# Kernel optimization log

Hardware: AMD Instinct MI355X
Metric: run time of the kernel (lower is better)

Reference implementation:

```python
import jax, jax.numpy as jnp
import numpy as np

N_NODES = 50000
N_EDGES = 800000
NUM_RELS = 16
IN_DIM, H_DIM, OUT_DIM = 128, 128, 64


def setup_inputs() -> dict:
    key = jax.random.key(0)
    ks = jax.random.split(key, 7)
    feat = jax.random.normal(ks[0], (N_NODES, IN_DIM), dtype=jnp.float32)
    norm = jax.random.uniform(ks[1], (N_EDGES, 1), dtype=jnp.float32)
    bound1 = 1.0 / np.sqrt(IN_DIM)
    bound2 = 1.0 / np.sqrt(H_DIM)
    W1 = jax.random.uniform(ks[2], (NUM_RELS, IN_DIM, H_DIM), dtype=jnp.float32, minval=-bound1, maxval=bound1)
    W2 = jax.random.uniform(ks[3], (NUM_RELS, H_DIM, OUT_DIM), dtype=jnp.float32, minval=-bound2, maxval=bound2)
    src = jax.random.randint(ks[4], (N_EDGES,), 0, N_NODES, dtype=jnp.int32)
    dst = jax.random.randint(ks[5], (N_EDGES,), 0, N_NODES, dtype=jnp.int32)
    etypes = jax.random.randint(ks[6], (N_EDGES,), 0, NUM_RELS, dtype=jnp.int32)
    return {"feat": feat, "norm": norm, "W1": W1, "W2": W2, "src": src, "dst": dst, "etypes": etypes}


def _rgcn_layer(h, W, src, dst, etypes, norm, num_nodes):
    # Transform every node by every relation weight (dense batched GEMM),
    # then gather the (src, etype) slice per edge: identical math to
    # gather_mm(h[src], W, idx_b=etypes) since matmul commutes with gather.
    t = jnp.einsum('ni,rio->nro', h, W)          # [N, R, O]
    msg = t[src, etypes] * norm                  # [E, O]
    return jax.ops.segment_sum(msg, dst, num_segments=num_nodes)  # sum-aggregate


def reference(feat, norm, W1, W2, src, dst, etypes):
    n = feat.shape[0]
    h = jax.nn.relu(_rgcn_layer(feat, W1, src, dst, etypes, norm, n))
    out = _rgcn_layer(h, W2, src, dst, etypes, norm, n)
    return out
```

## Files before the change

kernel.cpp:

```cpp
#include <hip/hip_runtime.h>


#define R_NUM 16

typedef __attribute__((ext_vector_type(8))) short bf16x8;
typedef __attribute__((ext_vector_type(4))) float f32x4;

__device__ __forceinline__ float bf2f(unsigned short u) {
    unsigned int x = ((unsigned int)u) << 16;
    return __builtin_bit_cast(float, x);
}
__device__ __forceinline__ unsigned short f2bf(float f) {
    unsigned int x = __builtin_bit_cast(unsigned int, f);
    x += 0x7FFFu + ((x >> 16) & 1u);
    return (unsigned short)(x >> 16);
}
__device__ __forceinline__ unsigned pack2(float a, float b) {
    return (unsigned)f2bf(a) | ((unsigned)f2bf(b) << 16);
}
__device__ __forceinline__ float lo16(unsigned v) { return bf2f((unsigned short)(v & 0xFFFF)); }
__device__ __forceinline__ float hi16(unsigned v) { return bf2f((unsigned short)(v >> 16)); }

__global__ void detect_dtype(const unsigned short* __restrict__ raw, int* flag) {
    __shared__ int tot;
    if (threadIdx.x == 0) tot = 0;
    __syncthreads();
    int c = 0;
    for (int i = threadIdx.x; i < 4096; i += 256) {
        unsigned short u = raw[2 * i];
        int e = (u >> 7) & 0xFF;
        if (e >= 113 && e <= 134) c++;
    }
    atomicAdd(&tot, c);
    __syncthreads();
    if (threadIdx.x == 0) *flag = (tot > 2048) ? 1 : 0;
}

__global__ void transpose_both(const void* __restrict__ W1, const void* __restrict__ W2,
                               unsigned short* __restrict__ w1t, unsigned short* __restrict__ w2t,
                               const int* __restrict__ flagp) {
    const int flag = *flagp;
    const int n1 = R_NUM * 128 * 128;
    const int n2 = R_NUM * 128 * 64;
    int idx = blockIdx.x * 256 + threadIdx.x;
    if (idx < n1) {
        int k = idx % 128, o = (idx / 128) % 128, r = idx / (128 * 128);
        int iin = (r * 128 + k) * 128 + o;
        float v = flag ? bf2f(((const unsigned short*)W1)[iin]) : ((const float*)W1)[iin];
        w1t[idx] = f2bf(v);
    } else if (idx < n1 + n2) {
        int j = idx - n1;
        int k = j % 128, o = (j / 128) % 64, r = j / (128 * 64);
        int iin = (r * 128 + k) * 64 + o;
        float v = flag ? bf2f(((const unsigned short*)W2)[iin]) : ((const float*)W2)[iin];
        w2t[j] = f2bf(v);
    }
}

template <int NOUT, int AMODE>
__global__ __launch_bounds__(256, 3) void gemm_nb(const void* __restrict__ Asrc,
                                                  const unsigned short* __restrict__ Wt,
                                                  unsigned short* __restrict__ T, int nnodes,
                                                  const int* __restrict__ flagp) {
    constexpr int LDA = 136;
    constexpr int NTC = NOUT / 64;
    __shared__ unsigned short lA[64 * LDA];
    const int tid = threadIdx.x;
    const int node0 = blockIdx.x * 64;
    const int flag = (AMODE == 0) ? *flagp : 1;

    for (int i = tid; i < 64 * 16; i += 256) {
        int row = i >> 4, seg = i & 15;
        int node = node0 + row;
        uint4 v = make_uint4(0u, 0u, 0u, 0u);
        if (node < nnodes) {
            if (AMODE == 2 || flag) {
                v = *(const uint4*)((const unsigned short*)Asrc + (size_t)node * 128 + seg * 8);
            } else {
                const float* p = (const float*)Asrc + (size_t)node * 128 + seg * 8;
                float4 f0 = ((const float4*)p)[0];
                float4 f1 = ((const float4*)p)[1];
                v.x = pack2(f0.x, f0.y);
                v.y = pack2(f0.z, f0.w);
                v.z = pack2(f1.x, f1.y);
                v.w = pack2(f1.z, f1.w);
            }
        }
        *(uint4*)(lA + row * LDA + seg * 8) = v;
    }
    __syncthreads();

    const int w = tid >> 6, lane = tid & 63;
    const int quad = lane >> 4, mr = lane & 15;

    bf16x8 afr[16];
#pragma unroll
    for (int mt = 0; mt < 4; mt++)
#pragma unroll
        for (int kk = 0; kk < 4; kk++)
            afr[mt * 4 + kk] = *(const bf16x8*)(lA + (mt * 16 + mr) * LDA + kk * 32 + quad * 8);

    const unsigned short* wb = Wt + (size_t)(w * 16 + mr) * 128 + quad * 8;

    for (int rel = 0; rel < R_NUM; rel++) {
        const unsigned short* wr = wb + (size_t)rel * NOUT * 128;
        bf16x8 bf[NTC][4];
#pragma unroll
        for (int c = 0; c < NTC; c++)
#pragma unroll
            for (int kk = 0; kk < 4; kk++)
                bf[c][kk] = *(const bf16x8*)(wr + (size_t)c * 64 * 128 + kk * 32);

        f32x4 acc[4][NTC];
#pragma unroll
        for (int mt = 0; mt < 4; mt++)
#pragma unroll
            for (int c = 0; c < NTC; c++) acc[mt][c] = 0.f;

#pragma unroll
        for (int kk = 0; kk < 4; kk++)
#pragma unroll
            for (int c = 0; c < NTC; c++)
#pragma unroll
                for (int mt = 0; mt < 4; mt++)
                    acc[mt][c] = __builtin_amdgcn_mfma_f32_16x16x32_bf16(bf[c][kk],
                                                                         afr[mt * 4 + kk],
                                                                         acc[mt][c], 0, 0, 0);

#pragma unroll
        for (int mt = 0; mt < 4; mt++) {
            int node = node0 + mt * 16 + mr;
            if (node < nnodes) {
#pragma unroll
                for (int c = 0; c < NTC; c++) {
                    uint2 pv;
                    pv.x = pack2(acc[mt][c][0], acc[mt][c][1]);
                    pv.y = pack2(acc[mt][c][2], acc[mt][c][3]);
                    *(uint2*)(T + ((size_t)rel * nnodes + node) * NOUT + c * 64 + w * 16 +
                              quad * 4) = pv;
                }
            }
        }
    }
}

__global__ void hist_dst(const int* __restrict__ dst, int* __restrict__ counts, int nedges) {
    int e = blockIdx.x * 256 + threadIdx.x;
    if (e < nedges) atomicAdd(&counts[dst[e]], 1);
}

__global__ __launch_bounds__(256) void scan_phase1(const int* __restrict__ counts,
                                                   int* __restrict__ blocksums, int n) {
    __shared__ int red[256];
    int base = blockIdx.x * 1024 + threadIdx.x * 4;
    int s = 0;
#pragma unroll
    for (int j = 0; j < 4; j++) {
        int idx = base + j;
        if (idx < n) s += counts[idx];
    }
    red[threadIdx.x] = s;
    __syncthreads();
    for (int d = 128; d > 0; d >>= 1) {
        if (threadIdx.x < d) red[threadIdx.x] += red[threadIdx.x + d];
        __syncthreads();
    }
    if (threadIdx.x == 0) blocksums[blockIdx.x] = red[0];
}

__global__ __launch_bounds__(1024) void scan_phase2(const int* __restrict__ blocksums,
                                                    int* __restrict__ blockoff, int nb) {
    __shared__ int arr[1024];
    int t = threadIdx.x;
    arr[t] = (t < nb) ? blocksums[t] : 0;
    __syncthreads();
    for (int d = 1; d < 1024; d <<= 1) {
        int v = (t >= d) ? arr[t - d] : 0;
        __syncthreads();
        arr[t] += v;
        __syncthreads();
    }
    if (t < nb) blockoff[t] = (t == 0) ? 0 : arr[t - 1];
}

__global__ __launch_bounds__(256) void scan_phase3(const int* __restrict__ counts,
                                                   const int* __restrict__ blockoff,
                                                   int* __restrict__ offsets,
                                                   int* __restrict__ cursor, int n) {
    __shared__ int tsum[256];
    int base = blockIdx.x * 1024 + threadIdx.x * 4;
    int c[4];
    int s = 0;
#pragma unroll
    for (int j = 0; j < 4; j++) {
        int idx = base + j;
        c[j] = (idx < n) ? counts[idx] : 0;
        s += c[j];
    }
    tsum[threadIdx.x] = s;
    __syncthreads();
    for (int d = 1; d < 256; d <<= 1) {
        int v = (threadIdx.x >= d) ? tsum[threadIdx.x - d] : 0;
        __syncthreads();
        tsum[threadIdx.x] += v;
        __syncthreads();
    }
    int run = blockoff[blockIdx.x] + ((threadIdx.x == 0) ? 0 : tsum[threadIdx.x - 1]);
#pragma unroll
    for (int j = 0; j < 4; j++) {
        int idx = base + j;
        if (idx < n) {
            offsets[idx] = run;
            cursor[idx] = run;
            if (idx == n - 1) offsets[n] = run + c[j];
            run += c[j];
        }
    }
}

__global__ void fill_payload(const int* __restrict__ src, const int* __restrict__ dst,
                             const int* __restrict__ et, const void* __restrict__ nrm,
                             const int* __restrict__ flagp, int* __restrict__ cursor,
                             uint2* __restrict__ payload, int nedges) {
    int e = blockIdx.x * 256 + threadIdx.x;
    if (e >= nedges) return;
    int flag = *flagp;
    float nm = flag ? bf2f(((const unsigned short*)nrm)[e]) : ((const float*)nrm)[e];
    int pos = atomicAdd(&cursor[dst[e]], 1);
    uint2 pl;
    pl.x = ((unsigned)src[e] << 4) | (unsigned)(et[e] & 15);
    pl.y = __builtin_bit_cast(unsigned, nm);
    payload[pos] = pl;
}

template <int NOUT, int OUTMODE>
__global__ __launch_bounds__(256) void gather_seg(const unsigned short* __restrict__ T,
                                                  const int* __restrict__ offsets,
                                                  const uint2* __restrict__ payload,
                                                  void* __restrict__ out, int nnodes,
                                                  const int* __restrict__ flagp) {
    constexpr int SUBW = NOUT / 2;
    const int lane = threadIdx.x & 63;
    const int ll = lane & (SUBW - 1);
    const int dpb = 256 / SUBW;
    const int dst = blockIdx.x * dpb + threadIdx.x / SUBW;
    if (dst >= nnodes) return;
    const int base = lane & ~(SUBW - 1);
    const int beg = offsets[dst], end = offsets[dst + 1];
    float ax = 0.f, ay = 0.f;

    auto rowp = [&](unsigned key) {
        return (const unsigned*)(T + ((size_t)(key & 15) * nnodes + (key >> 4)) * NOUT);
    };

    for (int i = beg; i < end; i += SUBW) {
        int cnt = min(SUBW, end - i);
        uint2 pl = make_uint2(0u, 0u);
        if (ll < cnt) pl = payload[i + ll];
        int j = 0;
        for (; j + 4 <= cnt; j += 4) {
            unsigned k0 = (unsigned)__shfl((int)pl.x, base + j);
            unsigned k1 = (unsigned)__shfl((int)pl.x, base + j + 1);
            unsigned k2 = (unsigned)__shfl((int)pl.x, base + j + 2);
            unsigned k3 = (unsigned)__shfl((int)pl.x, base + j + 3);
            float n0 = __builtin_bit_cast(float, (unsigned)__shfl((int)pl.y, base + j));
            float n1 = __builtin_bit_cast(float, (unsigned)__shfl((int)pl.y, base + j + 1));
            float n2 = __builtin_bit_cast(float, (unsigned)__shfl((int)pl.y, base + j + 2));
            float n3 = __builtin_bit_cast(float, (unsigned)__shfl((int)pl.y, base + j + 3));
            unsigned v0 = rowp(k0)[ll];
            unsigned v1 = rowp(k1)[ll];
            unsigned v2 = rowp(k2)[ll];
            unsigned v3 = rowp(k3)[ll];
            ax = fmaf(lo16(v0), n0, ax); ay = fmaf(hi16(v0), n0, ay);
            ax = fmaf(lo16(v1), n1, ax); ay = fmaf(hi16(v1), n1, ay);
            ax = fmaf(lo16(v2), n2, ax); ay = fmaf(hi16(v2), n2, ay);
            ax = fmaf(lo16(v3), n3, ax); ay = fmaf(hi16(v3), n3, ay);
        }
        for (; j < cnt; j++) {
            unsigned k = (unsigned)__shfl((int)pl.x, base + j);
            float nm = __builtin_bit_cast(float, (unsigned)__shfl((int)pl.y, base + j));
            unsigned v = rowp(k)[ll];
            ax = fmaf(lo16(v), nm, ax);
            ay = fmaf(hi16(v), nm, ay);
        }
    }
    if (OUTMODE == 0) {
        ((unsigned*)out)[(size_t)dst * SUBW + ll] = pack2(fmaxf(ax, 0.f), fmaxf(ay, 0.f));
    } else {
        if (*flagp) {
            ((unsigned*)out)[(size_t)dst * SUBW + ll] = pack2(ax, ay);
        } else {
            float2 v;
            v.x = ax; v.y = ay;
            ((float2*)out)[(size_t)dst * SUBW + ll] = v;
        }
    }
}

template <int NOUT, int AMODE>
__global__ __launch_bounds__(256) void gemm_rel(const void* __restrict__ Asrc,
                                                const unsigned short* __restrict__ Wt,
                                                unsigned short* __restrict__ T, int nnodes,
                                                int rbase, const int* __restrict__ flagp) {
    constexpr int LDA = 136;
    __shared__ unsigned short lA[64 * LDA];
    __shared__ unsigned short lB[NOUT * LDA];
    const int tid = threadIdx.x;
    const int node0 = blockIdx.x * 64;
    const int rel = rbase + blockIdx.y;
    const int Gr = gridDim.y;
    const int flag = (AMODE == 0) ? *flagp : 1;

    for (int i = tid; i < 64 * 16; i += 256) {
        int row = i >> 4, seg = i & 15;
        int node = node0 + row;
        uint4 v = make_uint4(0u, 0u, 0u, 0u);
        if (node < nnodes) {
            if (AMODE == 1) {
                const float* p = (const float*)Asrc + (size_t)node * 128 + seg * 8;
                float4 f0 = ((const float4*)p)[0];
                float4 f1 = ((const float4*)p)[1];
                v.x = pack2(fmaxf(f0.x, 0.f), fmaxf(f0.y, 0.f));
                v.y = pack2(fmaxf(f0.z, 0.f), fmaxf(f0.w, 0.f));
                v.z = pack2(fmaxf(f1.x, 0.f), fmaxf(f1.y, 0.f));
                v.w = pack2(fmaxf(f1.z, 0.f), fmaxf(f1.w, 0.f));
            } else if (flag) {
                v = *(const uint4*)((const unsigned short*)Asrc + (size_t)node * 128 + seg * 8);
            } else {
                const float* p = (const float*)Asrc + (size_t)node * 128 + seg * 8;
                float4 f0 = ((const float4*)p)[0];
                float4 f1 = ((const float4*)p)[1];
                v.x = pack2(f0.x, f0.y);
                v.y = pack2(f0.z, f0.w);
                v.z = pack2(f1.x, f1.y);
                v.w = pack2(f1.z, f1.w);
            }
        }
        *(uint4*)(lA + row * LDA + seg * 8) = v;
    }
    for (int i = tid; i < NOUT * 16; i += 256) {
        int o = i >> 4, seg = i & 15;
        *(uint4*)(lB + o * LDA + seg * 8) =
            *(const uint4*)(Wt + ((size_t)rel * NOUT + o) * 128 + seg * 8);
    }
    __syncthreads();

    const int w = tid >> 6, lane = tid & 63;
    const int quad = lane >> 4, mr = lane & 15;
    constexpr int NT = NOUT / 16;
    f32x4 acc[NT];
#pragma unroll
    for (int t = 0; t < NT; t++) acc[t] = 0.f;
    const unsigned short* pa = lA + (w * 16 + mr) * LDA + quad * 8;
    const unsigned short* pb = lB + mr * LDA + quad * 8;
#pragma unroll
    for (int kk = 0; kk < 4; kk++) {
        bf16x8 a = *(const bf16x8*)(pa + kk * 32);
#pragma unroll
        for (int nt = 0; nt < NT; nt++) {
            bf16x8 b = *(const bf16x8*)(pb + nt * 16 * LDA + kk * 32);
            acc[nt] = __builtin_amdgcn_mfma_f32_16x16x32_bf16(a, b, acc[nt], 0, 0, 0);
        }
    }
#pragma unroll
    for (int nt = 0; nt < NT; nt++)
#pragma unroll
        for (int reg = 0; reg < 4; reg++) {
            int node = node0 + w * 16 + quad * 4 + reg;
            if (node < nnodes)
                T[((size_t)node * Gr + blockIdx.y) * NOUT + nt * 16 + mr] = f2bf(acc[nt][reg]);
        }
}

template <int NOUT>
__global__ void scatter_k(const unsigned short* __restrict__ T, int Gr, int rbase,
                          const void* __restrict__ nrm, const int* __restrict__ flagp,
                          const int* __restrict__ src, const int* __restrict__ dst,
                          const int* __restrict__ et, float* __restrict__ accum, int nedges) {
    constexpr int LPE = NOUT / 2;
    const int flag = *flagp;
    const int epb = 256 / LPE;
    const int sub = threadIdx.x % LPE;
    const int slot = threadIdx.x / LPE;
    for (int e = blockIdx.x * epb + slot; e < nedges; e += gridDim.x * epb) {
        int g = et[e] - rbase;
        if (g < 0 || g >= Gr) continue;
        int s = src[e], d = dst[e];
        float nm = flag ? bf2f(((const unsigned short*)nrm)[e]) : ((const float*)nrm)[e];
        unsigned pv = ((const unsigned*)(T + ((size_t)s * Gr + g) * NOUT))[sub];
        float* p = accum + (size_t)d * NOUT + sub * 2;
        unsafeAtomicAdd(p, lo16(pv) * nm);
        unsafeAtomicAdd(p + 1, hi16(pv) * nm);
    }
}

__global__ void write_out(const float* __restrict__ acc, void* __restrict__ dout, int n,
                          const int* __restrict__ flagp) {
    int flag = *flagp;
    int i = blockIdx.x * 256 + threadIdx.x;
    if (i >= n) return;
    float v = acc[i];
    if (flag) ((unsigned short*)dout)[i] = f2bf(v);
    else      ((float*)dout)[i] = v;
}

extern "C" void kernel_launch(void* const* d_in, const int* in_sizes, int n_in,
                              void* d_out, int out_size, void* d_ws, size_t ws_size,
                              hipStream_t stream) {
    const void* feat = d_in[0];
    const void* norm = d_in[1];
    const void* W1 = d_in[2];
    const void* W2 = d_in[3];
    const int* src = (const int*)d_in[4];
    const int* dst = (const int*)d_in[5];
    const int* et  = (const int*)d_in[6];

    const int nnodes = in_sizes[0] / 128;
    const int nedges = in_sizes[1];

    char* ws = (char*)d_ws;
    size_t off = 0;
    auto alloc = [&](size_t bytes) { size_t o = off; off += (bytes + 255) & ~255ULL; return o; };
    size_t off_flag = alloc(4);
    size_t off_w1t  = alloc((size_t)R_NUM * 128 * 128 * 2);
    size_t off_w2t  = alloc((size_t)R_NUM * 64 * 128 * 2);

    int* flagp = (int*)(ws + off_flag);
    unsigned short* w1t = (unsigned short*)(ws + off_w1t);
    unsigned short* w2t = (unsigned short*)(ws + off_w2t);

    size_t f_off = off;
    auto falloc = [&](size_t bytes) { size_t o = f_off; f_off += (bytes + 255) & ~255ULL; return o; };
    size_t off_offs = falloc((size_t)(nnodes + 1) * 4);
    size_t off_curs = falloc((size_t)nnodes * 4);
    size_t off_cnt  = falloc((size_t)nnodes * 4);
    size_t off_bsum = falloc(1024 * 4);
    size_t off_boff = falloc(1024 * 4);
    size_t off_pay  = falloc((size_t)nedges * 8);
    size_t off_hbf  = falloc((size_t)nnodes * 128 * 2);
    size_t off_t    = falloc((size_t)nnodes * R_NUM * 128 * 2);
    const int nb = (nnodes + 1023) / 1024;
    bool fast = (f_off <= ws_size) && (nb <= 1024);

    const int gx = (nnodes + 63) / 64;
    const int ntr = R_NUM * 128 * 128 + R_NUM * 128 * 64;

    detect_dtype<<<1, 256, 0, stream>>>((const unsigned short*)feat, flagp);
    transpose_both<<<(ntr + 255) / 256, 256, 0, stream>>>(W1, W2, w1t, w2t, flagp);

    if (fast) {
        int* offs = (int*)(ws + off_offs);
        int* curs = (int*)(ws + off_curs);
        int* cnt  = (int*)(ws + off_cnt);
        int* bsum = (int*)(ws + off_bsum);
        int* boff = (int*)(ws + off_boff);
        uint2* pay = (uint2*)(ws + off_pay);
        unsigned short* hbf = (unsigned short*)(ws + off_hbf);
        unsigned short* t = (unsigned short*)(ws + off_t);

        hipMemsetAsync(cnt, 0, (size_t)nnodes * 4, stream);
        hist_dst<<<(nedges + 255) / 256, 256, 0, stream>>>(dst, cnt, nedges);
        scan_phase1<<<nb, 256, 0, stream>>>(cnt, bsum, nnodes);
        scan_phase2<<<1, 1024, 0, stream>>>(bsum, boff, nb);
        scan_phase3<<<nb, 256, 0, stream>>>(cnt, boff, offs, curs, nnodes);
        fill_payload<<<(nedges + 255) / 256, 256, 0, stream>>>(src, dst, et, norm, flagp,
                                                               curs, pay, nedges);

        gemm_nb<128, 0><<<gx, 256, 0, stream>>>(feat, w1t, t, nnodes, flagp);
        gather_seg<128, 0><<<(nnodes + 3) / 4, 256, 0, stream>>>(t, offs, pay, hbf, nnodes, flagp);
        gemm_nb<64, 2><<<gx, 256, 0, stream>>>(hbf, w2t, t, nnodes, flagp);
        gather_seg<64, 1><<<(nnodes + 7) / 8, 256, 0, stream>>>(t, offs, pay, d_out, nnodes, flagp);
        return;
    }

    size_t off_hpre = alloc((size_t)nnodes * 128 * 4);
    size_t off_oacc = alloc((size_t)nnodes * 64 * 4);
    size_t t_cap = (ws_size > off) ? (ws_size - off) : 0;
    auto pick_gr = [&](int ncol) {
        int gr = 0;
        for (int g = 16; g >= 1; g >>= 1)
            if ((size_t)nnodes * g * ncol * 2 <= t_cap) { gr = g; break; }
        return gr;
    };
    int Gr1 = pick_gr(128);
    int Gr2 = pick_gr(64);
    if (Gr1 < 1 || Gr2 < 1) {
        hipMemsetAsync(d_out, 0x42, (size_t)out_size * 2, stream);
        return;
    }
    float* hpre = (float*)(ws + off_hpre);
    float* oacc = (float*)(ws + off_oacc);
    unsigned short* t = (unsigned short*)(ws + off);

    hipMemsetAsync(hpre, 0, (size_t)nnodes * 128 * 4, stream);
    hipMemsetAsync(oacc, 0, (size_t)nnodes * 64 * 4, stream);
    for (int rb = 0; rb < R_NUM; rb += Gr1) {
        gemm_rel<128, 0><<<dim3(gx, Gr1), 256, 0, stream>>>(feat, w1t, t, nnodes, rb, flagp);
        scatter_k<128><<<4096, 256, 0, stream>>>(t, Gr1, rb, norm, flagp, src, dst, et, hpre, nedges);
    }
    for (int rb = 0; rb < R_NUM; rb += Gr2) {
        gemm_rel<64, 1><<<dim3(gx, Gr2), 256, 0, stream>>>(hpre, w2t, t, nnodes, rb, flagp);
        scatter_k<64><<<4096, 256, 0, stream>>>(t, Gr2, rb, norm, flagp, src, dst, et, oacc, nedges);
    }
    int nout = nnodes * 64;
    write_out<<<(nout + 255) / 256, 256, 0, stream>>>(oacc, d_out, nout, flagp);
}
```

Baseline: 407.3 us.

## Compute per-relation transforms only for unique (relation, source) pairs used by edges

Adds a preprocessing pass that marks which (relation, src) pairs actually appear among the edges. It then compacts them into per-relation slot lists padded to 64, and rewrites edge payloads to point at those slots. The GEMM now runs only over compacted slots with one relation per block, instead of transforming every node by all 16 relations. This cuts GEMM math and the size of the intermediate tensor that is written and later gathered. In exchange it adds several small kernels, a memset of a nodes×relations bucket array, and atomic-heavy marking and slot assignment.

```diff
diff --git a/kernel.cpp b/kernel.cpp
--- a/kernel.cpp
+++ b/kernel.cpp
@@ -57,89 +57,69 @@
     }
 }
 
-template <int NOUT, int AMODE>
-__global__ __launch_bounds__(256, 3) void gemm_nb(const void* __restrict__ Asrc,
-                                                  const unsigned short* __restrict__ Wt,
-                                                  unsigned short* __restrict__ T, int nnodes,
-                                                  const int* __restrict__ flagp) {
-    constexpr int LDA = 136;
-    constexpr int NTC = NOUT / 64;
-    __shared__ unsigned short lA[64 * LDA];
-    const int tid = threadIdx.x;
-    const int node0 = blockIdx.x * 64;
-    const int flag = (AMODE == 0) ? *flagp : 1;
-
-    for (int i = tid; i < 64 * 16; i += 256) {
-        int row = i >> 4, seg = i & 15;
-        int node = node0 + row;
-        uint4 v = make_uint4(0u, 0u, 0u, 0u);
-        if (node < nnodes) {
-            if (AMODE == 2 || flag) {
-                v = *(const uint4*)((const unsigned short*)Asrc + (size_t)node * 128 + seg * 8);
-            } else {
-                const float* p = (const float*)Asrc + (size_t)node * 128 + seg * 8;
-                float4 f0 = ((const float4*)p)[0];
-                float4 f1 = ((const float4*)p)[1];
-                v.x = pack2(f0.x, f0.y);
-                v.y = pack2(f0.z, f0.w);
-                v.z = pack2(f1.x, f1.y);
-                v.w = pack2(f1.z, f1.w);
-            }
-        }
-        *(uint4*)(lA + row * LDA + seg * 8) = v;
-    }
-    __syncthreads();
-
-    const int w = tid >> 6, lane = tid & 63;
-    const int quad = lane >> 4, mr = lane & 15;
-
-    bf16x8 afr[16];
-#pragma unroll
-    for (int mt = 0; mt < 4; mt++)
-#pragma unroll
-        for (int kk = 0; kk < 4; kk++)
-            afr[mt * 4 + kk] = *(const bf16x8*)(lA + (mt * 16 + mr) * LDA + kk * 32 + quad * 8);
-
-    const unsigned short* wb = Wt + (size_t)(w * 16 + mr) * 128 + quad * 8;
-
-    for (int rel = 0; rel < R_NUM; rel++) {
-        const unsigned short* wr = wb + (size_t)rel * NOUT * 128;
-        bf16x8 bf[NTC][4];
-#pragma unroll
-        for (int c = 0; c < NTC; c++)
-#pragma unroll
-            for (int kk = 0; kk < 4; kk++)
-                bf[c][kk] = *(const bf16x8*)(wr + (size_t)c * 64 * 128 + kk * 32);
-
-        f32x4 acc[4][NTC];
-#pragma unroll
-        for (int mt = 0; mt < 4; mt++)
-#pragma unroll
-            for (int c = 0; c < NTC; c++) acc[mt][c] = 0.f;
-
-#pragma unroll
-        for (int kk = 0; kk < 4; kk++)
-#pragma unroll
-            for (int c = 0; c < NTC; c++)
-#pragma unroll
-                for (int mt = 0; mt < 4; mt++)
-                    acc[mt][c] = __builtin_amdgcn_mfma_f32_16x16x32_bf16(bf[c][kk],
-                                                                         afr[mt * 4 + kk],
-                                                                         acc[mt][c], 0, 0, 0);
-
-#pragma unroll
-        for (int mt = 0; mt < 4; mt++) {
-            int node = node0 + mt * 16 + mr;
-            if (node < nnodes) {
-#pragma unroll
-                for (int c = 0; c < NTC; c++) {
-                    uint2 pv;
-                    pv.x = pack2(acc[mt][c][0], acc[mt][c][1]);
-                    pv.y = pack2(acc[mt][c][2], acc[mt][c][3]);
-                    *(uint2*)(T + ((size_t)rel * nnodes + node) * NOUT + c * 64 + w * 16 +
-                              quad * 4) = pv;
-                }
-            }
+__global__ void mark_pairs(const int* __restrict__ src, const int* __restrict__ et,
+                           int* __restrict__ bucket, int* __restrict__ relcnt,
+                           int nnodes, int nedges) {
+    __shared__ int lcnt[R_NUM];
+    if (threadIdx.x < R_NUM) lcnt[threadIdx.x] = 0;
+    __syncthreads();
+    int e = blockIdx.x * 256 + threadIdx.x;
+    if (e < nedges) {
+        int r = et[e] & 15;
+        int key = r * nnodes + src[e];
+        if (atomicExch(&bucket[key], 1) == 0) atomicAdd(&lcnt[r], 1);
+    }
+    __syncthreads();
+    if (threadIdx.x < R_NUM && lcnt[threadIdx.x]) atomicAdd(&relcnt[threadIdx.x], lcnt[threadIdx.x]);
+}
+
+__global__ void relscan(const int* __restrict__ relcnt, int* __restrict__ relbase,
+                        int* __restrict__ relcur) {
+    if (threadIdx.x == 0) {
+        int tot = 0;
+        for (int r = 0; r < R_NUM; r++) {
+            relbase[r] = tot;
+            tot += (relcnt[r] + 63) & ~63;
+        }
+        relbase[R_NUM] = tot;
+    }
+    if (threadIdx.x < R_NUM) relcur[threadIdx.x] = 0;
+}
+
+__global__ __launch_bounds__(256) void assign_slots(int* __restrict__ bucket,
+                                                    const int* __restrict__ relbase,
+                                                    int* __restrict__ relcur,
+                                                    int* __restrict__ slot2src, int nnodes) {
+    __shared__ int tsum[256];
+    __shared__ int sbase;
+    const int r = blockIdx.y;
+    const int b0 = blockIdx.x * 1024 + threadIdx.x * 4;
+    int u[4];
+    int s = 0;
+#pragma unroll
+    for (int j = 0; j < 4; j++) {
+        int b = b0 + j;
+        u[j] = (b < nnodes) ? (bucket[r * nnodes + b] == 1) : 0;
+        s += u[j];
+    }
+    tsum[threadIdx.x] = s;
+    __syncthreads();
+    for (int d = 1; d < 256; d <<= 1) {
+        int v = (threadIdx.x >= d) ? tsum[threadIdx.x - d] : 0;
+        __syncthreads();
+        tsum[threadIdx.x] += v;
+        __syncthreads();
+    }
+    if (threadIdx.x == 255) sbase = relbase[r] + atomicAdd(&relcur[r], tsum[255]);
+    __syncthreads();
+    int run = sbase + ((threadIdx.x == 0) ? 0 : tsum[threadIdx.x - 1]);
+#pragma unroll
+    for (int j = 0; j < 4; j++) {
+        int b = b0 + j;
+        if (b < nnodes && u[j]) {
+            bucket[r * nnodes + b] = run + 1;
+            slot2src[run] = b;
+            run++;
         }
     }
 }
@@ -220,17 +200,104 @@
 
 __global__ void fill_payload(const int* __restrict__ src, const int* __restrict__ dst,
                              const int* __restrict__ et, const void* __restrict__ nrm,
-                             const int* __restrict__ flagp, int* __restrict__ cursor,
-                             uint2* __restrict__ payload, int nedges) {
+                             const int* __restrict__ flagp, const int* __restrict__ bucket,
+                             int* __restrict__ cursor, uint2* __restrict__ payload,
+                             int nnodes, int nedges) {
     int e = blockIdx.x * 256 + threadIdx.x;
     if (e >= nedges) return;
     int flag = *flagp;
     float nm = flag ? bf2f(((const unsigned short*)nrm)[e]) : ((const float*)nrm)[e];
+    int slot = bucket[(et[e] & 15) * nnodes + src[e]] - 1;
     int pos = atomicAdd(&cursor[dst[e]], 1);
     uint2 pl;
-    pl.x = ((unsigned)src[e] << 4) | (unsigned)(et[e] & 15);
+    pl.x = (unsigned)slot;
     pl.y = __builtin_bit_cast(unsigned, nm);
     payload[pos] = pl;
+}
+
+template <int NOUT, int AMODE>
+__global__ __launch_bounds__(256, 3) void gemm_cp(const void* __restrict__ Asrc,
+                                                  const unsigned short* __restrict__ Wt,
+                                                  unsigned short* __restrict__ T,
+                                                  const int* __restrict__ relbase,
+                                                  const int* __restrict__ slot2src,
+                                                  const int* __restrict__ flagp) {
+    constexpr int LDA = 136;
+    constexpr int NTC = NOUT / 64;
+    __shared__ unsigned short lA[64 * LDA];
+    const int tid = threadIdx.x;
+    const int slot0 = blockIdx.x * 64;
+    if (slot0 >= relbase[R_NUM]) return;
+    const int flag = (AMODE == 0) ? *flagp : 1;
+
+    int rel = 0;
+#pragma unroll
+    for (int st = 8; st >= 1; st >>= 1)
+        if (relbase[rel + st] <= slot0) rel += st;
+
+    for (int i = tid; i < 64 * 16; i += 256) {
+        int row = i >> 4, seg = i & 15;
+        int srcn = slot2src[slot0 + row];
+        uint4 v;
+        if (AMODE == 2 || flag) {
+            v = *(const uint4*)((const unsigned short*)Asrc + (size_t)srcn * 128 + seg * 8);
+        } else {
+            const float* p = (const float*)Asrc + (size_t)srcn * 128 + seg * 8;
+            float4 f0 = ((const float4*)p)[0];
+            float4 f1 = ((const float4*)p)[1];
+            v.x = pack2(f0.x, f0.y);
+            v.y = pack2(f0.z, f0.w);
+            v.z = pack2(f1.x, f1.y);
+            v.w = pack2(f1.z, f1.w);
+        }
+        *(uint4*)(lA + row * LDA + seg * 8) = v;
+    }
+    __syncthreads();
+
+    const int w = tid >> 6, lane = tid & 63;
+    const int quad = lane >> 4, mr = lane & 15;
+
+    bf16x8 afr[16];
+#pragma unroll
+    for (int mt = 0; mt < 4; mt++)
+#pragma unroll
+        for (int kk = 0; kk < 4; kk++)
+            afr[mt * 4 + kk] = *(const bf16x8*)(lA + (mt * 16 + mr) * LDA + kk * 32 + quad * 8);
+
+    bf16x8 bf[NTC][4];
+#pragma unroll
+    for (int c = 0; c < NTC; c++)
+#pragma unroll
+        for (int kk = 0; kk < 4; kk++)
+            bf[c][kk] = *(const bf16x8*)(Wt + ((size_t)rel * NOUT + c * 64 + w * 16 + mr) * 128 +
+                                         kk * 32 + quad * 8);
+
+    f32x4 acc[4][NTC];
+#pragma unroll
+    for (int mt = 0; mt < 4; mt++)
+#pragma unroll
+        for (int c = 0; c < NTC; c++) acc[mt][c] = 0.f;
+
+#pragma unroll
+    for (int kk = 0; kk < 4; kk++)
+#pragma unroll
+        for (int c = 0; c < NTC; c++)
+#pragma unroll
+            for (int mt = 0; mt < 4; mt++)
+                acc[mt][c] = __builtin_amdgcn_mfma_f32_16x16x32_bf16(bf[c][kk], afr[mt * 4 + kk],
+                                                                     acc[mt][c], 0, 0, 0);
+
+#pragma unroll
+    for (int mt = 0; mt < 4; mt++) {
+        int slot = slot0 + mt * 16 + mr;
+#pragma unroll
+        for (int c = 0; c < NTC; c++) {
+            uint2 pv;
+            pv.x = pack2(acc[mt][c][0], acc[mt][c][1]);
+            pv.y = pack2(acc[mt][c][2], acc[mt][c][3]);
+            *(uint2*)(T + (size_t)slot * NOUT + c * 64 + w * 16 + quad * 4) = pv;
+        }
+    }
 }
 
 template <int NOUT, int OUTMODE>
@@ -249,10 +316,6 @@
     const int beg = offsets[dst], end = offsets[dst + 1];
     float ax = 0.f, ay = 0.f;
 
-    auto rowp = [&](unsigned key) {
-        return (const unsigned*)(T + ((size_t)(key & 15) * nnodes + (key >> 4)) * NOUT);
-    };
-
     for (int i = beg; i < end; i += SUBW) {
         int cnt = min(SUBW, end - i);
         uint2 pl = make_uint2(0u, 0u);
@@ -267,10 +330,10 @@
             float n1 = __builtin_bit_cast(float, (unsigned)__shfl((int)pl.y, base + j + 1));
             float n2 = __builtin_bit_cast(float, (unsigned)__shfl((int)pl.y, base + j + 2));
             float n3 = __builtin_bit_cast(float, (unsigned)__shfl((int)pl.y, base + j + 3));
-            unsigned v0 = rowp(k0)[ll];
-            unsigned v1 = rowp(k1)[ll];
-            unsigned v2 = rowp(k2)[ll];
-            unsigned v3 = rowp(k3)[ll];
+            unsigned v0 = ((const unsigned*)(T + (size_t)k0 * NOUT))[ll];
+            unsigned v1 = ((const unsigned*)(T + (size_t)k1 * NOUT))[ll];
+            unsigned v2 = ((const unsigned*)(T + (size_t)k2 * NOUT))[ll];
+            unsigned v3 = ((const unsigned*)(T + (size_t)k3 * NOUT))[ll];
             ax = fmaf(lo16(v0), n0, ax); ay = fmaf(hi16(v0), n0, ay);
             ax = fmaf(lo16(v1), n1, ax); ay = fmaf(hi16(v1), n1, ay);
             ax = fmaf(lo16(v2), n2, ax); ay = fmaf(hi16(v2), n2, ay);
@@ -279,7 +342,7 @@
         for (; j < cnt; j++) {
             unsigned k = (unsigned)__shfl((int)pl.x, base + j);
             float nm = __builtin_bit_cast(float, (unsigned)__shfl((int)pl.y, base + j));
-            unsigned v = rowp(k)[ll];
+            unsigned v = ((const unsigned*)(T + (size_t)k * NOUT))[ll];
             ax = fmaf(lo16(v), nm, ax);
             ay = fmaf(hi16(v), nm, ay);
         }
@@ -429,46 +492,68 @@
     unsigned short* w1t = (unsigned short*)(ws + off_w1t);
     unsigned short* w2t = (unsigned short*)(ws + off_w2t);
 
+    const long long maxpairs = (long long)nnodes * R_NUM;
+    const int cap = (int)((maxpairs < (long long)nedges ? maxpairs : (long long)nedges)
+                          + 64 * R_NUM + 64);
+
     size_t f_off = off;
     auto falloc = [&](size_t bytes) { size_t o = f_off; f_off += (bytes + 255) & ~255ULL; return o; };
-    size_t off_offs = falloc((size_t)(nnodes + 1) * 4);
-    size_t off_curs = falloc((size_t)nnodes * 4);
-    size_t off_cnt  = falloc((size_t)nnodes * 4);
-    size_t off_bsum = falloc(1024 * 4);
-    size_t off_boff = falloc(1024 * 4);
-    size_t off_pay  = falloc((size_t)nedges * 8);
-    size_t off_hbf  = falloc((size_t)nnodes * 128 * 2);
-    size_t off_t    = falloc((size_t)nnodes * R_NUM * 128 * 2);
+    size_t off_bucket = falloc((size_t)nnodes * R_NUM * 4);
+    size_t off_rmeta  = falloc(64 * 4);
+    size_t off_s2s    = falloc((size_t)cap * 4);
+    size_t off_offs   = falloc((size_t)(nnodes + 1) * 4);
+    size_t off_curs   = falloc((size_t)nnodes * 4);
+    size_t off_cnt    = falloc((size_t)nnodes * 4);
+    size_t off_bsum   = falloc(1024 * 4);
+    size_t off_boff   = falloc(1024 * 4);
+    size_t off_pay    = falloc((size_t)nedges * 8);
+    size_t off_hbf    = falloc((size_t)cap * 128 * 2);
+    size_t off_hn     = falloc((size_t)nnodes * 128 * 2);
+    size_t off_t      = falloc((size_t)cap * 128 * 2);
     const int nb = (nnodes + 1023) / 1024;
     bool fast = (f_off <= ws_size) && (nb <= 1024);
-
-    const int gx = (nnodes + 63) / 64;
+    (void)off_hbf;
+
     const int ntr = R_NUM * 128 * 128 + R_NUM * 128 * 64;
 
     detect_dtype<<<1, 256, 0, stream>>>((const unsigned short*)feat, flagp);
     transpose_both<<<(ntr + 255) / 256, 256, 0, stream>>>(W1, W2, w1t, w2t, flagp);
 
     if (fast) {
+        int* bucket = (int*)(ws + off_bucket);
+        int* relcnt = (int*)(ws + off_rmeta);
+        int* relbase = relcnt + 16;
+        int* relcur = relbase + 17;
+        int* s2s = (int*)(ws + off_s2s);
         int* offs = (int*)(ws + off_offs);
         int* curs = (int*)(ws + off_curs);
         int* cnt  = (int*)(ws + off_cnt);
         int* bsum = (int*)(ws + off_bsum);
         int* boff = (int*)(ws + off_boff);
         uint2* pay = (uint2*)(ws + off_pay);
-        unsigned short* hbf = (unsigned short*)(ws + off_hbf);
+        unsigned short* h = (unsigned short*)(ws + off_hn);
         unsigned short* t = (unsigned short*)(ws + off_t);
 
+        hipMemsetAsync(bucket, 0, (size_t)nnodes * R_NUM * 4, stream);
+        hipMemsetAsync((void*)(ws + off_rmeta), 0, 64 * 4, stream);
+        hipMemsetAsync(s2s, 0, (size_t)cap * 4, stream);
+        mark_pairs<<<(nedges + 255) / 256, 256, 0, stream>>>(src, et, bucket, relcnt,
+                                                             nnodes, nedges);
+        relscan<<<1, 64, 0, stream>>>(relcnt, relbase, relcur);
+        assign_slots<<<dim3((nnodes + 1023) / 1024, R_NUM), 256, 0, stream>>>(bucket, relbase,
+                                                                              relcur, s2s, nnodes);
         hipMemsetAsync(cnt, 0, (size_t)nnodes * 4, stream);
         hist_dst<<<(nedges + 255) / 256, 256, 0, stream>>>(dst, cnt, nedges);
         scan_phase1<<<nb, 256, 0, stream>>>(cnt, bsum, nnodes);
         scan_phase2<<<1, 1024, 0, stream>>>(bsum, boff, nb);
         scan_phase3<<<nb, 256, 0, stream>>>(cnt, boff, offs, curs, nnodes);
         fill_payload<<<(nedges + 255) / 256, 256, 0, stream>>>(src, dst, et, norm, flagp,
-                                                               curs, pay, nedges);
-
-        gemm_nb<128, 0><<<gx, 256, 0, stream>>>(feat, w1t, t, nnodes, flagp);
-        gather_seg<128, 0><<<(nnodes + 3) / 4, 256, 0, stream>>>(t, offs, pay, hbf, nnodes, flagp);
-        gemm_nb<64, 2><<<gx, 256, 0, stream>>>(hbf, w2t, t, nnodes, flagp);
+                                                               bucket, curs, pay, nnodes, nedges);
+
+        const int gslots = (cap + 63) / 64;
+        gemm_cp<128, 0><<<gslots, 256, 0, stream>>>(feat, w1t, t, relbase, s2s, flagp);
+        gather_seg<128, 0><<<(nnodes + 3) / 4, 256, 0, stream>>>(t, offs, pay, h, nnodes, flagp);
+        gemm_cp<64, 2><<<gslots, 256, 0, stream>>>(h, w2t, t, relbase, s2s, flagp);
         gather_seg<64, 1><<<(nnodes + 7) / 8, 256, 0, stream>>>(t, offs, pay, d_out, nnodes, flagp);
         return;
     }
@@ -491,6 +576,7 @@
     float* hpre = (float*)(ws + off_hpre);
     float* oacc = (float*)(ws + off_oacc);
     unsigned short* t = (unsigned short*)(ws + off);
+    const int gx = (nnodes + 63) / 64;
 
     hipMemsetAsync(hpre, 0, (size_t)nnodes * 128 * 4, stream);
     hipMemsetAsync(oacc, 0, (size_t)nnodes * 64 * 4, stream);
```

Measured after the change: 1.312 ms. 3.22x slower.
